# Kernel optimization log

Hardware: AMD Instinct MI355X
Metric: run time of the kernel (lower is better)

Reference implementation:

```python
import jax, jax.numpy as jnp
import numpy as np

N_NODES = 50000
N_EDGES = 800000
X_DIM = 32
E_DIM = 32
HID = 64
OUT = 32


def setup_inputs() -> dict:
    key = jax.random.key(0)
    ks = jax.random.split(key, 6)
    x = jax.random.normal(ks[0], (N_NODES, X_DIM), dtype=jnp.float32)
    edge_index = jax.random.randint(ks[1], (2, N_EDGES), 0, N_NODES, dtype=jnp.int64)
    edge_attr = jax.random.normal(ks[2], (N_EDGES, E_DIM), dtype=jnp.float32)
    in_dim = 2 * X_DIM + E_DIM  # 96
    W1 = jax.random.normal(ks[3], (in_dim, HID), dtype=jnp.float32) * (1.0 / np.sqrt(in_dim))
    b1 = jnp.zeros((HID,), dtype=jnp.float32)
    W2 = jax.random.normal(ks[4], (HID, OUT), dtype=jnp.float32) * (1.0 / np.sqrt(HID))
    b2 = jnp.zeros((OUT,), dtype=jnp.float32)
    return {"x": x, "edge_index": edge_index, "edge_attr": edge_attr,
            "W1": W1, "b1": b1, "W2": W2, "b2": b2}


def reference(x, edge_index, edge_attr, W1, b1, W2, b2):
    num_nodes = x.shape[0]
    rol, col = edge_index[0], edge_index[1]
    # gather endpoint features + edge attr -> [E, 2*x_dim + e_dim]
    e_feat = jnp.concatenate([x[rol], x[col], edge_attr], axis=-1)
    # 2-layer MLP (ReLU hidden)
    h = jax.nn.relu(e_feat @ W1 + b1)
    v = h @ W2 + b2  # [E, OUT]
    # scatter-max aggregation into destination nodes (empty segments -> -inf)
    x_cand = jax.ops.segment_max(v, col, num_segments=num_nodes)
    # elementwise max residual against trailing slice of x
    return jnp.maximum(x_cand, x[:, -v.shape[-1]:])
```

## Files before the change

### kernel.cpp

```cpp
#include <hip/hip_runtime.h>


constexpr int XD   = 32;
constexpr int HID  = 64;
constexpr int OUTD = 32;
constexpr int BM   = 128;
constexpr int HSTR = 72;
constexpr int BIN_SHIFT = 5;
constexpr int BINW  = 1 << BIN_SHIFT;
constexpr int CAPB  = 1024;
constexpr int BLK_E = 8192;
constexpr int EPB   = BLK_E / 256;

typedef __attribute__((ext_vector_type(8)))  short    short8;
typedef __attribute__((ext_vector_type(4)))  float    f32x4;
typedef __attribute__((ext_vector_type(4)))  float    floatx4;
typedef __attribute__((ext_vector_type(2)))  unsigned u32x2;

static __device__ __forceinline__ unsigned f2bf(float f) {
    union { float f; unsigned u; } x; x.f = f;
    unsigned r = x.u + 0x7fff + ((x.u >> 16) & 1);
    return r >> 16;
}
static __device__ __forceinline__ unsigned encf(float f) {
    unsigned u = __float_as_uint(f);
    return (u >> 31) ? ~u : (u | 0x80000000u);
}
static __device__ __forceinline__ float decf(unsigned k) {
    return __uint_as_float((k >> 31) ? (k & 0x7fffffffu) : ~k);
}

__global__ __launch_bounds__(256) void prep_hist(
    const float* __restrict__ x, unsigned* __restrict__ xbf,
    const float* __restrict__ W1, const float* __restrict__ W2,
    unsigned* __restrict__ w1s, unsigned* __restrict__ w2s,
    const int* __restrict__ ei, unsigned* __restrict__ cnt,
    int n_edges, int nbins, int nblk, int total8)
{
    __shared__ unsigned lh[2048];
    const int t = threadIdx.x;
    const int b = blockIdx.x;

    if (b < nblk) {
        for (int i = t; i < nbins; i += 256) lh[i] = 0u;
        __syncthreads();
        const int chunk = b * BLK_E;
#pragma unroll
        for (int i = 0; i < EPB; ++i) {
            const int e = chunk + i * 256 + t;
            if (e < n_edges)
                atomicAdd(&lh[((unsigned)ei[n_edges + e]) >> BIN_SHIFT], 1u);
        }
        __syncthreads();
        for (int i = t; i < nbins; i += 256)
            cnt[(size_t)b * nbins + i] = lh[i];
        return;
    }

    const int i = (b - nblk) * 256 + t;

    if (i < total8) {
        const float4* src = reinterpret_cast<const float4*>(x) + (size_t)i * 2;
        float4 a = src[0], bb = src[1];
        uint4 o;
        o.x = f2bf(a.x)  | (f2bf(a.y)  << 16);
        o.y = f2bf(a.z)  | (f2bf(a.w)  << 16);
        o.z = f2bf(bb.x) | (f2bf(bb.y) << 16);
        o.w = f2bf(bb.z) | (f2bf(bb.w) << 16);
        reinterpret_cast<uint4*>(xbf)[i] = o;
    }

    if (i < 768) {
        const int ti = i >> 6, lane = i & 63;
        const int nt = ti / 3, ks = ti % 3;
        const int col = nt * 16 + (lane & 15);
        const int k0  = ks * 32 + ((lane >> 4) << 3);
        unsigned o[4];
#pragma unroll
        for (int p = 0; p < 4; ++p)
            o[p] = f2bf(W1[(k0 + 2 * p) * HID + col]) |
                   (f2bf(W1[(k0 + 2 * p + 1) * HID + col]) << 16);
        reinterpret_cast<uint4*>(w1s)[i] = make_uint4(o[0], o[1], o[2], o[3]);
    } else if (i < 1024) {
        const int tt = i - 768;
        const int ti = tt >> 6, lane = tt & 63;
        const int nt = ti >> 1, ks = ti & 1;
        const int col = nt * 16 + (lane & 15);
        const int k0  = ks * 32 + ((lane >> 4) << 3);
        unsigned o[4];
#pragma unroll
        for (int p = 0; p < 4; ++p)
            o[p] = f2bf(W2[(k0 + 2 * p) * OUTD + col]) |
                   (f2bf(W2[(k0 + 2 * p + 1) * OUTD + col]) << 16);
        reinterpret_cast<uint4*>(w2s)[tt] = make_uint4(o[0], o[1], o[2], o[3]);
    }
}

__global__ __launch_bounds__(128) void bin_off(
    const unsigned* __restrict__ cnt, unsigned* __restrict__ off,
    unsigned* __restrict__ totals, int nblk, int nbins)
{
    __shared__ unsigned ts[128];
    const int j = blockIdx.x;
    const int t = threadIdx.x;
    const unsigned d = (t < nblk) ? cnt[(size_t)t * nbins + j] : 0u;
    ts[t] = d;
    __syncthreads();
#pragma unroll
    for (int o = 1; o < 128; o <<= 1) {
        unsigned v = (t >= o) ? ts[t - o] : 0u;
        __syncthreads();
        ts[t] += v;
        __syncthreads();
    }
    if (t < nblk) off[(size_t)t * nbins + j] = ts[t] - d;
    if (t == 127) totals[j] = ts[127];
}

__global__ __launch_bounds__(256) void bin_write(
    const int* __restrict__ ei, const unsigned* __restrict__ off,
    unsigned* __restrict__ rec,
    int n_edges, int nbins)
{
    __shared__ unsigned loff[2048];
    __shared__ unsigned lrank[2048];
    const int t = threadIdx.x;
    const int b = blockIdx.x;
    for (int i = t; i < nbins; i += 256) {
        loff[i]  = (unsigned)i * CAPB + off[(size_t)b * nbins + i];
        lrank[i] = 0u;
    }
    __syncthreads();
    const int chunk = b * BLK_E;
#pragma unroll
    for (int i = 0; i < EPB; ++i) {
        const int e = chunk + i * 256 + t;
        if (e < n_edges) {
            const unsigned row = (unsigned)ei[e];
            const unsigned col = (unsigned)ei[n_edges + e];
            const unsigned bin = col >> BIN_SHIFT;
            const unsigned r   = atomicAdd(&lrank[bin], 1u);
            const unsigned pos = loff[bin] + r;
            u32x2 v; v.x = (row << 16) | col; v.y = (unsigned)e;
            *reinterpret_cast<u32x2*>(rec + (size_t)pos * 2) = v;
        }
    }
}

__global__ __launch_bounds__(256) void edge_mlp_fused(
    const unsigned* __restrict__ xbf,
    const unsigned* __restrict__ rec,
    const float*    __restrict__ ea,
    const unsigned* __restrict__ w1s,
    const unsigned* __restrict__ w2s,
    const float*    __restrict__ b1,
    const float*    __restrict__ b2,
    const float*    __restrict__ x,
    const unsigned* __restrict__ totals,
    float*          __restrict__ out,
    int n_edges, int n_nodes)
{
    __shared__ alignas(16) unsigned short Hlds[4 * 16 * HSTR];
    __shared__ unsigned accK[BINW * OUTD];

    const int t    = threadIdx.x;
    const int lane = t & 63;
    const int wave = t >> 6;
    const int bin  = blockIdx.x;
    const int n0   = bin << BIN_SHIFT;

    const unsigned sbeg = (unsigned)bin * CAPB;
    unsigned tot = totals[bin];
    if (tot > CAPB) tot = CAPB;
    const unsigned send = sbeg + tot;

    const unsigned* w1p = w1s + (size_t)lane * 4;
    const unsigned* w2p = w2s + (size_t)lane * 4;

    float bb1[4];
#pragma unroll
    for (int nt = 0; nt < 4; ++nt) bb1[nt] = b1[nt * 16 + (lane & 15)];
    float bb2[2];
#pragma unroll
    for (int nt = 0; nt < 2; ++nt) bb2[nt] = b2[nt * 16 + (lane & 15)];

#pragma unroll
    for (int k = 0; k < (BINW * OUTD) / 256; ++k) {
        const int idx = t + k * 256;
        const int g   = n0 + (idx >> 5);
        const float r = (g < n_nodes) ? x[(size_t)g * XD + (idx & 31)] : 0.0f;
        accK[idx] = encf(r);
    }
    __syncthreads();

    const int ntile = (int)(tot + BM - 1) / BM;
    const int koff  = lane >> 4;
    const int hbase = wave * 16;

    for (int tile = 0; tile < ntile; ++tile) {
        unsigned qx = 0u, qy = 0u;
        if (lane < 32) {
            unsigned p = sbeg + (unsigned)tile * BM + (unsigned)wave * 32 + (unsigned)lane;
            if (p >= send) p = send - 1;
            const u32x2 q = __builtin_nontemporal_load(
                reinterpret_cast<const u32x2*>(rec + (size_t)p * 2));
            qx = q.x; qy = q.y;
        }

#pragma unroll
        for (int mi = 0; mi < 2; ++mi) {
            const int s = mi * 16 + (lane & 15);
            const unsigned rcp = (unsigned)__shfl((int)qx, s, 64);
            const unsigned eid = (unsigned)__shfl((int)qy, s, 64);
            const unsigned idR = rcp >> 16;
            const unsigned idC = rcp & 0xffffu;

            const short8 aR = *reinterpret_cast<const short8*>(
                xbf + (size_t)idR * 16 + koff * 4);
            const short8 aC = *reinterpret_cast<const short8*>(
                xbf + (size_t)idC * 16 + koff * 4);
            const floatx4* ep = reinterpret_cast<const floatx4*>(
                ea + (size_t)eid * 32 + koff * 8);
            const floatx4 e0 = __builtin_nontemporal_load(ep);
            const floatx4 e1 = __builtin_nontemporal_load(ep + 1);
            union { uint4 u; short8 s8; } ae;
            ae.u.x = f2bf(e0.x) | (f2bf(e0.y) << 16);
            ae.u.y = f2bf(e0.z) | (f2bf(e0.w) << 16);
            ae.u.z = f2bf(e1.x) | (f2bf(e1.y) << 16);
            ae.u.w = f2bf(e1.z) | (f2bf(e1.w) << 16);

            f32x4 acc1[4];
#pragma unroll
            for (int nt = 0; nt < 4; ++nt) acc1[nt] = (f32x4){0.f, 0.f, 0.f, 0.f};
#pragma unroll
            for (int nt = 0; nt < 4; ++nt) {
                const short8 wA = *reinterpret_cast<const short8*>(w1p + (size_t)(nt * 3 + 0) * 256);
                const short8 wB = *reinterpret_cast<const short8*>(w1p + (size_t)(nt * 3 + 1) * 256);
                const short8 wE = *reinterpret_cast<const short8*>(w1p + (size_t)(nt * 3 + 2) * 256);
                acc1[nt] = __builtin_amdgcn_mfma_f32_16x16x32_bf16(aR,    wA, acc1[nt], 0, 0, 0);
                acc1[nt] = __builtin_amdgcn_mfma_f32_16x16x32_bf16(aC,    wB, acc1[nt], 0, 0, 0);
                acc1[nt] = __builtin_amdgcn_mfma_f32_16x16x32_bf16(ae.s8, wE, acc1[nt], 0, 0, 0);
            }

#pragma unroll
            for (int nt = 0; nt < 4; ++nt)
#pragma unroll
                for (int r = 0; r < 4; ++r) {
                    const float h = fmaxf(acc1[nt][r] + bb1[nt], 0.0f);
                    Hlds[(hbase + ((lane >> 4) << 2) + r) * HSTR + nt * 16 + (lane & 15)] =
                        (unsigned short)f2bf(h);
                }

            f32x4 acc2[2];
#pragma unroll
            for (int nt = 0; nt < 2; ++nt) acc2[nt] = (f32x4){0.f, 0.f, 0.f, 0.f};
#pragma unroll
            for (int ks = 0; ks < 2; ++ks) {
                const short8 hfrag = *reinterpret_cast<const short8*>(
                    &Hlds[(hbase + (lane & 15)) * HSTR + ks * 32 + ((lane >> 4) << 3)]);
#pragma unroll
                for (int nt = 0; nt < 2; ++nt) {
                    const short8 wF = *reinterpret_cast<const short8*>(w2p + (size_t)(nt * 2 + ks) * 256);
                    acc2[nt] = __builtin_amdgcn_mfma_f32_16x16x32_bf16(hfrag, wF, acc2[nt], 0, 0, 0);
                }
            }

#pragma unroll
            for (int r = 0; r < 4; ++r) {
                const int rowl = mi * 16 + ((lane >> 4) << 2) + r;
                const unsigned rcp2 = (unsigned)__shfl((int)qx, rowl, 64);
                const int ln = (int)(rcp2 & 0xffffu) - n0;
#pragma unroll
                for (int nt = 0; nt < 2; ++nt) {
                    const float val = acc2[nt][r] + bb2[nt];
                    atomicMax(&accK[ln * OUTD + nt * 16 + (lane & 15)], encf(val));
                }
            }
        }
    }

    __syncthreads();
#pragma unroll
    for (int k = 0; k < (BINW * OUTD) / 256; ++k) {
        const int idx = t + k * 256;
        const int g   = n0 + (idx >> 5);
        if (g < n_nodes)
            out[(size_t)g * OUTD + (idx & 31)] = decf(accK[idx]);
    }
}

extern "C" void kernel_launch(void* const* d_in, const int* in_sizes, int n_in,
                              void* d_out, int out_size, void* d_ws, size_t ws_size,
                              hipStream_t stream)
{
    const float* x  = (const float*)d_in[0];
    const int*   ei = (const int*)  d_in[1];
    const float* ea = (const float*)d_in[2];
    const float* W1 = (const float*)d_in[3];
    const float* b1 = (const float*)d_in[4];
    const float* W2 = (const float*)d_in[5];
    const float* b2 = (const float*)d_in[6];
    float* out = (float*)d_out;

    const int n_nodes = in_sizes[0] / XD;
    const int n_edges = in_sizes[2] / 32;
    const int nbins   = (n_nodes + BINW - 1) >> BIN_SHIFT;
    const int nblk    = (n_edges + BLK_E - 1) / BLK_E;

    size_t off_b = 0;
    unsigned* cnt    = (unsigned*)((char*)d_ws + off_b); off_b += (size_t)nblk * nbins * 4;
    unsigned* offm   = (unsigned*)((char*)d_ws + off_b); off_b += (size_t)nblk * nbins * 4;
    unsigned* totals = (unsigned*)((char*)d_ws + off_b); off_b += (size_t)nbins * 4;
    off_b = (off_b + 63) & ~(size_t)63;
    unsigned* rec    = (unsigned*)((char*)d_ws + off_b); off_b += (size_t)nbins * CAPB * 8;
    unsigned* xbf    = (unsigned*)((char*)d_ws + off_b); off_b += (size_t)n_nodes * 16 * 4;
    unsigned* w1s    = (unsigned*)((char*)d_ws + off_b); off_b += 768 * 16;
    unsigned* w2s    = (unsigned*)((char*)d_ws + off_b);

    const int total8     = n_nodes * XD / 8;
    const int prep_blk   = (max(total8, 1024) + 255) / 256;

    prep_hist<<<nblk + prep_blk, 256, 0, stream>>>(
        x, xbf, W1, W2, w1s, w2s, ei, cnt, n_edges, nbins, nblk, total8);
    bin_off<<<nbins, 128, 0, stream>>>(cnt, offm, totals, nblk, nbins);
    bin_write<<<nblk, 256, 0, stream>>>(ei, offm, rec, n_edges, nbins);
    edge_mlp_fused<<<nbins, 256, 0, stream>>>(
        xbf, rec, ea, w1s, w2s, b1, b2, x, totals, out, n_edges, n_nodes);
}
```

Measured before the change: 95.41 us.

## Replace destination binning with direct global atomicMax into encoded output

Drops the histogram, offset-scan and bin-write passes that grouped edges by destination node. Edges are now processed in their original order: each tile reads edge_index directly, and the MLP results are merged with global atomicMax into an order-preserving integer encoding of the output, which is first initialised from x and decoded in a final pass. This removes three kernel launches and the record buffer traffic. In exchange it issues many scattered global atomics instead of LDS atomics, and the edge_attr reads become streaming rather than permuted.

New measurement: 115.5 us. 1.21x slower.

```diff
diff --git a/kernel.cpp b/kernel.cpp
--- a/kernel.cpp
+++ b/kernel.cpp
@@ -5,17 +5,12 @@
 constexpr int HID  = 64;
 constexpr int OUTD = 32;
 constexpr int BM   = 128;
+constexpr int EPT  = 512;
 constexpr int HSTR = 72;
-constexpr int BIN_SHIFT = 5;
-constexpr int BINW  = 1 << BIN_SHIFT;
-constexpr int CAPB  = 1024;
-constexpr int BLK_E = 8192;
-constexpr int EPB   = BLK_E / 256;
 
 typedef __attribute__((ext_vector_type(8)))  short    short8;
 typedef __attribute__((ext_vector_type(4)))  float    f32x4;
 typedef __attribute__((ext_vector_type(4)))  float    floatx4;
-typedef __attribute__((ext_vector_type(2)))  unsigned u32x2;
 
 static __device__ __forceinline__ unsigned f2bf(float f) {
     union { float f; unsigned u; } x; x.f = f;
@@ -30,34 +25,21 @@
     return __uint_as_float((k >> 31) ? (k & 0x7fffffffu) : ~k);
 }
 
-__global__ __launch_bounds__(256) void prep_hist(
-    const float* __restrict__ x, unsigned* __restrict__ xbf,
+__global__ __launch_bounds__(256) void prep(
+    const float* __restrict__ x, unsigned* __restrict__ outE,
+    unsigned* __restrict__ xbf,
     const float* __restrict__ W1, const float* __restrict__ W2,
     unsigned* __restrict__ w1s, unsigned* __restrict__ w2s,
-    const int* __restrict__ ei, unsigned* __restrict__ cnt,
-    int n_edges, int nbins, int nblk, int total8)
-{
-    __shared__ unsigned lh[2048];
-    const int t = threadIdx.x;
-    const int b = blockIdx.x;
-
-    if (b < nblk) {
-        for (int i = t; i < nbins; i += 256) lh[i] = 0u;
-        __syncthreads();
-        const int chunk = b * BLK_E;
-#pragma unroll
-        for (int i = 0; i < EPB; ++i) {
-            const int e = chunk + i * 256 + t;
-            if (e < n_edges)
-                atomicAdd(&lh[((unsigned)ei[n_edges + e]) >> BIN_SHIFT], 1u);
-        }
-        __syncthreads();
-        for (int i = t; i < nbins; i += 256)
-            cnt[(size_t)b * nbins + i] = lh[i];
-        return;
-    }
-
-    const int i = (b - nblk) * 256 + t;
+    int total4, int total8)
+{
+    const int i = blockIdx.x * 256 + threadIdx.x;
+
+    if (i < total4) {
+        const float4 a = reinterpret_cast<const float4*>(x)[i];
+        uint4 o;
+        o.x = encf(a.x); o.y = encf(a.y); o.z = encf(a.z); o.w = encf(a.w);
+        reinterpret_cast<uint4*>(outE)[i] = o;
+    }
 
     if (i < total8) {
         const float4* src = reinterpret_cast<const float4*>(x) + (size_t)i * 2;
@@ -96,83 +78,23 @@
     }
 }
 
-__global__ __launch_bounds__(128) void bin_off(
-    const unsigned* __restrict__ cnt, unsigned* __restrict__ off,
-    unsigned* __restrict__ totals, int nblk, int nbins)
-{
-    __shared__ unsigned ts[128];
-    const int j = blockIdx.x;
-    const int t = threadIdx.x;
-    const unsigned d = (t < nblk) ? cnt[(size_t)t * nbins + j] : 0u;
-    ts[t] = d;
-    __syncthreads();
-#pragma unroll
-    for (int o = 1; o < 128; o <<= 1) {
-        unsigned v = (t >= o) ? ts[t - o] : 0u;
-        __syncthreads();
-        ts[t] += v;
-        __syncthreads();
-    }
-    if (t < nblk) off[(size_t)t * nbins + j] = ts[t] - d;
-    if (t == 127) totals[j] = ts[127];
-}
-
-__global__ __launch_bounds__(256) void bin_write(
-    const int* __restrict__ ei, const unsigned* __restrict__ off,
-    unsigned* __restrict__ rec,
-    int n_edges, int nbins)
-{
-    __shared__ unsigned loff[2048];
-    __shared__ unsigned lrank[2048];
-    const int t = threadIdx.x;
-    const int b = blockIdx.x;
-    for (int i = t; i < nbins; i += 256) {
-        loff[i]  = (unsigned)i * CAPB + off[(size_t)b * nbins + i];
-        lrank[i] = 0u;
-    }
-    __syncthreads();
-    const int chunk = b * BLK_E;
-#pragma unroll
-    for (int i = 0; i < EPB; ++i) {
-        const int e = chunk + i * 256 + t;
-        if (e < n_edges) {
-            const unsigned row = (unsigned)ei[e];
-            const unsigned col = (unsigned)ei[n_edges + e];
-            const unsigned bin = col >> BIN_SHIFT;
-            const unsigned r   = atomicAdd(&lrank[bin], 1u);
-            const unsigned pos = loff[bin] + r;
-            u32x2 v; v.x = (row << 16) | col; v.y = (unsigned)e;
-            *reinterpret_cast<u32x2*>(rec + (size_t)pos * 2) = v;
-        }
-    }
-}
-
-__global__ __launch_bounds__(256) void edge_mlp_fused(
+__global__ __launch_bounds__(256) void edge_mlp_atomic(
     const unsigned* __restrict__ xbf,
-    const unsigned* __restrict__ rec,
+    const int*      __restrict__ ei,
     const float*    __restrict__ ea,
     const unsigned* __restrict__ w1s,
     const unsigned* __restrict__ w2s,
     const float*    __restrict__ b1,
     const float*    __restrict__ b2,
-    const float*    __restrict__ x,
-    const unsigned* __restrict__ totals,
-    float*          __restrict__ out,
-    int n_edges, int n_nodes)
+    unsigned*       __restrict__ outE,
+    int n_edges)
 {
     __shared__ alignas(16) unsigned short Hlds[4 * 16 * HSTR];
-    __shared__ unsigned accK[BINW * OUTD];
 
     const int t    = threadIdx.x;
     const int lane = t & 63;
     const int wave = t >> 6;
-    const int bin  = blockIdx.x;
-    const int n0   = bin << BIN_SHIFT;
-
-    const unsigned sbeg = (unsigned)bin * CAPB;
-    unsigned tot = totals[bin];
-    if (tot > CAPB) tot = CAPB;
-    const unsigned send = sbeg + tot;
+    const int base = blockIdx.x * EPT;
 
     const unsigned* w1p = w1s + (size_t)lane * 4;
     const unsigned* w2p = w2s + (size_t)lane * 4;
@@ -184,43 +106,39 @@
 #pragma unroll
     for (int nt = 0; nt < 2; ++nt) bb2[nt] = b2[nt * 16 + (lane & 15)];
 
-#pragma unroll
-    for (int k = 0; k < (BINW * OUTD) / 256; ++k) {
-        const int idx = t + k * 256;
-        const int g   = n0 + (idx >> 5);
-        const float r = (g < n_nodes) ? x[(size_t)g * XD + (idx & 31)] : 0.0f;
-        accK[idx] = encf(r);
-    }
-    __syncthreads();
-
-    const int ntile = (int)(tot + BM - 1) / BM;
     const int koff  = lane >> 4;
     const int hbase = wave * 16;
 
-    for (int tile = 0; tile < ntile; ++tile) {
-        unsigned qx = 0u, qy = 0u;
+#pragma unroll 1
+    for (int tile = 0; tile < EPT / BM; ++tile) {
+        const int tbase = base + tile * BM;
+        if (tbase >= n_edges) break;
+
+        unsigned qx = 0u;
         if (lane < 32) {
-            unsigned p = sbeg + (unsigned)tile * BM + (unsigned)wave * 32 + (unsigned)lane;
-            if (p >= send) p = send - 1;
-            const u32x2 q = __builtin_nontemporal_load(
-                reinterpret_cast<const u32x2*>(rec + (size_t)p * 2));
-            qx = q.x; qy = q.y;
+            int e = tbase + wave * 32 + lane;
+            if (e >= n_edges) e = n_edges - 1;
+            const unsigned row = (unsigned)ei[e];
+            const unsigned col = (unsigned)ei[n_edges + e];
+            qx = (row << 16) | col;
         }
 
 #pragma unroll
         for (int mi = 0; mi < 2; ++mi) {
             const int s = mi * 16 + (lane & 15);
             const unsigned rcp = (unsigned)__shfl((int)qx, s, 64);
-            const unsigned eid = (unsigned)__shfl((int)qy, s, 64);
             const unsigned idR = rcp >> 16;
             const unsigned idC = rcp & 0xffffu;
+
+            int e_slot = tbase + wave * 32 + s;
+            if (e_slot >= n_edges) e_slot = n_edges - 1;
 
             const short8 aR = *reinterpret_cast<const short8*>(
                 xbf + (size_t)idR * 16 + koff * 4);
             const short8 aC = *reinterpret_cast<const short8*>(
                 xbf + (size_t)idC * 16 + koff * 4);
             const floatx4* ep = reinterpret_cast<const floatx4*>(
-                ea + (size_t)eid * 32 + koff * 8);
+                ea + (size_t)e_slot * 32 + koff * 8);
             const floatx4 e0 = __builtin_nontemporal_load(ep);
             const floatx4 e1 = __builtin_nontemporal_load(ep + 1);
             union { uint4 u; short8 s8; } ae;
@@ -269,23 +187,25 @@
             for (int r = 0; r < 4; ++r) {
                 const int rowl = mi * 16 + ((lane >> 4) << 2) + r;
                 const unsigned rcp2 = (unsigned)__shfl((int)qx, rowl, 64);
-                const int ln = (int)(rcp2 & 0xffffu) - n0;
+                const unsigned col  = rcp2 & 0xffffu;
 #pragma unroll
                 for (int nt = 0; nt < 2; ++nt) {
                     const float val = acc2[nt][r] + bb2[nt];
-                    atomicMax(&accK[ln * OUTD + nt * 16 + (lane & 15)], encf(val));
+                    atomicMax(outE + (size_t)col * OUTD + nt * 16 + (lane & 15), encf(val));
                 }
             }
         }
     }
-
-    __syncthreads();
-#pragma unroll
-    for (int k = 0; k < (BINW * OUTD) / 256; ++k) {
-        const int idx = t + k * 256;
-        const int g   = n0 + (idx >> 5);
-        if (g < n_nodes)
-            out[(size_t)g * OUTD + (idx & 31)] = decf(accK[idx]);
+}
+
+__global__ __launch_bounds__(256) void decode_out(unsigned* __restrict__ outE, int total4)
+{
+    const int i = blockIdx.x * 256 + threadIdx.x;
+    if (i < total4) {
+        uint4 v = reinterpret_cast<const uint4*>(outE)[i];
+        float4 o;
+        o.x = decf(v.x); o.y = decf(v.y); o.z = decf(v.z); o.w = decf(v.w);
+        reinterpret_cast<float4*>(outE)[i] = o;
     }
 }
 
@@ -300,30 +220,23 @@
     const float* b1 = (const float*)d_in[4];
     const float* W2 = (const float*)d_in[5];
     const float* b2 = (const float*)d_in[6];
-    float* out = (float*)d_out;
+    unsigned* outE = (unsigned*)d_out;
 
     const int n_nodes = in_sizes[0] / XD;
     const int n_edges = in_sizes[2] / 32;
-    const int nbins   = (n_nodes + BINW - 1) >> BIN_SHIFT;
-    const int nblk    = (n_edges + BLK_E - 1) / BLK_E;
 
     size_t off_b = 0;
-    unsigned* cnt    = (unsigned*)((char*)d_ws + off_b); off_b += (size_t)nblk * nbins * 4;
-    unsigned* offm   = (unsigned*)((char*)d_ws + off_b); off_b += (size_t)nblk * nbins * 4;
-    unsigned* totals = (unsigned*)((char*)d_ws + off_b); off_b += (size_t)nbins * 4;
-    off_b = (off_b + 63) & ~(size_t)63;
-    unsigned* rec    = (unsigned*)((char*)d_ws + off_b); off_b += (size_t)nbins * CAPB * 8;
-    unsigned* xbf    = (unsigned*)((char*)d_ws + off_b); off_b += (size_t)n_nodes * 16 * 4;
-    unsigned* w1s    = (unsigned*)((char*)d_ws + off_b); off_b += 768 * 16;
-    unsigned* w2s    = (unsigned*)((char*)d_ws + off_b);
-
-    const int total8     = n_nodes * XD / 8;
-    const int prep_blk   = (max(total8, 1024) + 255) / 256;
-
-    prep_hist<<<nblk + prep_blk, 256, 0, stream>>>(
-        x, xbf, W1, W2, w1s, w2s, ei, cnt, n_edges, nbins, nblk, total8);
-    bin_off<<<nbins, 128, 0, stream>>>(cnt, offm, totals, nblk, nbins);
-    bin_write<<<nblk, 256, 0, stream>>>(ei, offm, rec, n_edges, nbins);
-    edge_mlp_fused<<<nbins, 256, 0, stream>>>(
-        xbf, rec, ea, w1s, w2s, b1, b2, x, totals, out, n_edges, n_nodes);
-}
+    unsigned* xbf = (unsigned*)((char*)d_ws + off_b); off_b += (size_t)n_nodes * 16 * 4;
+    unsigned* w1s = (unsigned*)((char*)d_ws + off_b); off_b += 768 * 16;
+    unsigned* w2s = (unsigned*)((char*)d_ws + off_b);
+
+    const int total4 = n_nodes * OUTD / 4;
+    const int total8 = n_nodes * XD / 8;
+    const int prep_grid = (max(total4, max(total8, 1024)) + 255) / 256;
+    const int edge_grid = (n_edges + EPT - 1) / EPT;
+
+    prep<<<prep_grid, 256, 0, stream>>>(x, outE, xbf, W1, W2, w1s, w2s, total4, total8);
+    edge_mlp_atomic<<<edge_grid, 256, 0, stream>>>(
+        xbf, ei, ea, w1s, w2s, b1, b2, outE, n_edges);
+    decode_out<<<(total4 + 255) / 256, 256, 0, stream>>>(outE, total4);
+}
```
